# Kernel optimization log

Measured on AMD Instinct MI355X. Metric: run time of the kernel, lower is better.

The kernel has to match this reference:

```python
import jax, jax.numpy as jnp
import numpy as np

N, NODE_DIM, EDGE_DIM, HID, NREL = 1024, 128, 32, 128, 16


def _sage(h, adj, W, b):
    # agg = mean over (weighted) neighbors: (adj @ h) / (deg + 1e-6)
    agg = (adj @ h) / (jnp.sum(adj, axis=1, keepdims=True) + 1e-6)
    return jax.nn.relu(jnp.concatenate([h, agg], axis=1) @ W.T + b)


def setup_inputs() -> dict:
    key = jax.random.key(0)
    ks = jax.random.split(key, 12)
    s1 = 1.0 / np.sqrt(2 * NODE_DIM)
    s2 = 1.0 / np.sqrt(2 * HID)
    s3 = 1.0 / np.sqrt(2 * HID + EDGE_DIM)
    s4 = 1.0 / np.sqrt(HID)
    return {
        "node_feat": jax.random.normal(ks[0], (N, NODE_DIM), jnp.float32),
        "edge_feat": jax.random.normal(ks[1], (N, N, EDGE_DIM), jnp.float32),
        "adj": jax.random.uniform(ks[2], (N, N), jnp.float32),
        "W_g1": jax.random.normal(ks[3], (HID, 2 * NODE_DIM), jnp.float32) * s1,
        "b_g1": jax.random.normal(ks[4], (HID,), jnp.float32) * s1,
        "W_g2": jax.random.normal(ks[5], (HID, 2 * HID), jnp.float32) * s2,
        "b_g2": jax.random.normal(ks[6], (HID,), jnp.float32) * s2,
        "W_c1": jax.random.normal(ks[7], (HID, 2 * HID + EDGE_DIM), jnp.float32) * s3,
        "b_c1": jax.random.normal(ks[8], (HID,), jnp.float32) * s3,
        "W_c2": jax.random.normal(ks[9], (NREL, HID), jnp.float32) * s4,
        "b_c2": jax.random.normal(ks[10], (NREL,), jnp.float32) * s4,
    }


def reference(node_feat, edge_feat, adj, W_g1, b_g1, W_g2, b_g2, W_c1, b_c1, W_c2, b_c2):
    h = _sage(node_feat, adj, W_g1, b_g1)          # [N, HID]
    h = _sage(h, adj, W_g2, b_g2)                  # [N, HID]
    H = h.shape[1]
    # Split first classifier layer over [h_i ; h_j ; e_ij] to avoid a huge concat.
    Wa, Wb, We = W_c1[:, :H], W_c1[:, H:2 * H], W_c1[:, 2 * H:]
    pre = ((h @ Wa.T)[:, None, :]
           + (h @ Wb.T)[None, :, :]
           + jnp.einsum('ije,he->ijh', edge_feat, We)
           + b_c1)                                  # [N, N, HID]
    logits = jax.nn.relu(pre) @ W_c2.T + b_c2       # [N, N, NREL]
    # diagonal (i == j) stays zero, matching the skipped loop iterations
    n = logits.shape[0]
    mask = 1.0 - jnp.eye(n, dtype=logits.dtype)
    return logits * mask[:, :, None]
```

## Files before the change

### kernel.cpp

```cpp
#include <hip/hip_runtime.h>
#include <hip/hip_bf16.h>
#include <stdint.h>

constexpr int NN = 1024;
constexpr int DD = 128;
constexpr int EDIM = 32;
constexpr int NR = 16;

using short4v = __attribute__((ext_vector_type(4))) short;
using short8v = __attribute__((ext_vector_type(8))) short;
using f32x4   = __attribute__((ext_vector_type(4))) float;

__device__ __forceinline__ short f2bf(float x) {
  __hip_bfloat16 h = __float2bfloat16(x);
  return __builtin_bit_cast(short, h);
}

__device__ __forceinline__ void nt_store4(float* p, const float4& v) {
  f32x4 t;
  t[0] = v.x; t[1] = v.y; t[2] = v.z; t[3] = v.w;
  __builtin_nontemporal_store(t, (f32x4*)p);
}

__device__ __forceinline__ void gl_lds16(const void* g, void* l) {
  __builtin_amdgcn_global_load_lds(
      (const __attribute__((address_space(1))) unsigned int*)(uintptr_t)g,
      (__attribute__((address_space(3))) unsigned int*)(uint32_t)(uintptr_t)l,
      16, 0, 0);
}

__global__ __launch_bounds__(256) void k_adjgemm(const float* __restrict__ adj,
                                                 const float* __restrict__ X,
                                                 float* __restrict__ part) {
  __shared__ float sadj[16][136];
  int t = threadIdx.x;
  int ic = blockIdx.x & 63, kc = blockIdx.x >> 6;
  int i0 = ic * 16, k0 = kc * 128;
  {
    int il = t >> 4;
    int kl = (t & 15) * 8;
    const float4* src = (const float4*)(adj + (size_t)(i0 + il) * NN + k0 + kl);
    *(float4*)&sadj[il][kl]     = src[0];
    *(float4*)&sadj[il][kl + 4] = src[1];
  }
  __syncthreads();
  int hq = (t & 31) * 4;
  int ir = t >> 5;
  float4 acc0 = {0,0,0,0}, acc1 = {0,0,0,0};
  const float* Xb = X + (size_t)k0 * DD + hq;
  #pragma unroll 4
  for (int k = 0; k < 128; ++k) {
    float4 xv = *(const float4*)(Xb + (size_t)k * DD);
    float a0 = sadj[ir][k];
    float a1 = sadj[ir + 8][k];
    acc0.x += a0 * xv.x; acc0.y += a0 * xv.y; acc0.z += a0 * xv.z; acc0.w += a0 * xv.w;
    acc1.x += a1 * xv.x; acc1.y += a1 * xv.y; acc1.z += a1 * xv.z; acc1.w += a1 * xv.w;
  }
  *(float4*)(part + ((size_t)kc * NN + (i0 + ir)) * DD + hq)     = acc0;
  *(float4*)(part + ((size_t)kc * NN + (i0 + ir + 8)) * DD + hq) = acc1;
}

__global__ __launch_bounds__(256) void k_dense1(const float* __restrict__ X,
                                                const float* __restrict__ part,
                                                const float* __restrict__ adj,
                                                const float* __restrict__ W,
                                                const float* __restrict__ b,
                                                float* __restrict__ out,
                                                float* __restrict__ rsinv) {
  __shared__ float sagg[2][128];
  __shared__ float red[4];
  int t = threadIdx.x;
  int ig = t >> 7, h = t & 127;
  int i = blockIdx.x * 2 + ig;
  {
    const float4* ar = (const float4*)(adj + (size_t)i * NN);
    float4 v0 = ar[h * 2], v1 = ar[h * 2 + 1];
    float s = v0.x + v0.y + v0.z + v0.w + v1.x + v1.y + v1.z + v1.w;
    #pragma unroll
    for (int off = 32; off > 0; off >>= 1) s += __shfl_down(s, off, 64);
    if ((t & 63) == 0) red[t >> 6] = s;
  }
  __syncthreads();
  float rs = 1.0f / (red[ig * 2] + red[ig * 2 + 1] + 1e-6f);
  if (h == 0) rsinv[i] = rs;
  {
    float ss = 0.f;
    #pragma unroll
    for (int kc = 0; kc < 8; ++kc) ss += part[(size_t)kc * NN * DD + (size_t)i * DD + h];
    sagg[ig][h] = ss * rs;
  }
  __syncthreads();
  const float4* xr = (const float4*)(X + (size_t)i * DD);
  const float4* ar = (const float4*)(&sagg[ig][0]);
  const float4* w1 = (const float4*)(W + (size_t)h * 256);
  const float4* w2 = (const float4*)(W + (size_t)h * 256 + DD);
  float acc = b[h];
  #pragma unroll 8
  for (int k = 0; k < 32; ++k) {
    float4 x = xr[k], w = w1[k];
    acc += x.x * w.x + x.y * w.y + x.z * w.z + x.w * w.w;
  }
  #pragma unroll 8
  for (int k = 0; k < 32; ++k) {
    float4 y = ar[k], w = w2[k];
    acc += y.x * w.x + y.y * w.y + y.z * w.z + y.w * w.w;
  }
  out[(size_t)i * DD + h] = fmaxf(acc, 0.f);
}

__global__ __launch_bounds__(256) void k_dense2ab(const float* __restrict__ X,
                                                  const float* __restrict__ part,
                                                  const float* __restrict__ rsinv,
                                                  const float* __restrict__ W,
                                                  const float* __restrict__ b,
                                                  const float* __restrict__ Wc1,
                                                  const float* __restrict__ bc1,
                                                  float* __restrict__ Aib,
                                                  float* __restrict__ Bmat) {
  __shared__ float sagg[2][128];
  __shared__ float sh2[2][128];
  int t = threadIdx.x;
  int ig = t >> 7, h = t & 127;
  int i = blockIdx.x * 2 + ig;
  {
    float ss = 0.f;
    #pragma unroll
    for (int kc = 0; kc < 8; ++kc) ss += part[(size_t)kc * NN * DD + (size_t)i * DD + h];
    sagg[ig][h] = ss * rsinv[i];
  }
  __syncthreads();
  {
    const float4* xr = (const float4*)(X + (size_t)i * DD);
    const float4* ar = (const float4*)(&sagg[ig][0]);
    const float4* w1 = (const float4*)(W + (size_t)h * 256);
    const float4* w2 = (const float4*)(W + (size_t)h * 256 + DD);
    float acc = b[h];
    #pragma unroll 8
    for (int k = 0; k < 32; ++k) {
      float4 x = xr[k], w = w1[k];
      acc += x.x * w.x + x.y * w.y + x.z * w.z + x.w * w.w;
    }
    #pragma unroll 8
    for (int k = 0; k < 32; ++k) {
      float4 y = ar[k], w = w2[k];
      acc += y.x * w.x + y.y * w.y + y.z * w.z + y.w * w.w;
    }
    sh2[ig][h] = fmaxf(acc, 0.f);
  }
  __syncthreads();
  const float4* xr = (const float4*)(&sh2[ig][0]);
  const float4* wa = (const float4*)(Wc1 + (size_t)h * 288);
  const float4* wb = (const float4*)(Wc1 + (size_t)h * 288 + 128);
  float aa = bc1[h], bb = 0.f;
  #pragma unroll 8
  for (int k = 0; k < 32; ++k) {
    float4 x = xr[k];
    float4 a = wa[k], b2 = wb[k];
    aa += x.x * a.x + x.y * a.y + x.z * a.z + x.w * a.w;
    bb += x.x * b2.x + x.y * b2.y + x.z * b2.z + x.w * b2.w;
  }
  Aib[(size_t)i * DD + h] = aa;
  Bmat[(size_t)i * DD + h] = bb;
}


#define EDGE_BODY(T, OFF, VMN, PF) do {                                       \
    float4 e0_, e1_;                                                          \
    asm volatile("s_waitcnt vmcnt(" #VMN ")\n\t"                              \
                 "ds_read_b128 %0, %2 offset:" #OFF "\n\t"                    \
                 "ds_read_b128 %1, %3 offset:" #OFF "\n\t"                    \
                 "s_waitcnt lgkmcnt(0)"                                       \
                 : "=&v"(e0_), "=&v"(e1_)                                     \
                 : "v"(ea0), "v"(ea1)                                         \
                 : "memory");                                                 \
    __builtin_amdgcn_sched_barrier(0);                                        \
    if (PF) {                                                                 \
      const char* src_ = ebl + (size_t)((T) + 5) * 131072;                    \
      gl_lds16(src_, esw + (OFF));                                            \
      gl_lds16(src_ + 1024, esw + (OFF) + 1024);                              \
    }                                                                         \
    __builtin_amdgcn_sched_barrier(0);                                        \
    short8v ef_;                                                              \
    ef_[0]=f2bf(e0_.x); ef_[1]=f2bf(e0_.y); ef_[2]=f2bf(e0_.z); ef_[3]=f2bf(e0_.w); \
    ef_[4]=f2bf(e1_.x); ef_[5]=f2bf(e1_.y); ef_[6]=f2bf(e1_.z); ef_[7]=f2bf(e1_.w); \
    char* pw_ = psm + (((T) & 1) << 12);                                      \
    const float* ap_ = aibs + (T) * 128 + 4 * g;                              \
    _Pragma("unroll")                                                         \
    for (int n = 0; n < 8; ++n) {                                             \
      float4 av_ = *(const float4*)(ap_ + 16 * n);                            \
      f32x4 ci_;                                                              \
      ci_[0] = av_.x + bjv[n].x; ci_[1] = av_.y + bjv[n].y;                   \
      ci_[2] = av_.z + bjv[n].z; ci_[3] = av_.w + bjv[n].w;                   \
      f32x4 acc_ = __builtin_amdgcn_mfma_f32_16x16x32_bf16(weF[n], ef_, ci_, 0, 0, 0); \
      short4v pk_;                                                            \
      pk_[0] = f2bf(fmaxf(acc_[0], 0.f)); pk_[1] = f2bf(fmaxf(acc_[1], 0.f)); \
      pk_[2] = f2bf(fmaxf(acc_[2], 0.f)); pk_[3] = f2bf(fmaxf(acc_[3], 0.f)); \
      *(short4v*)(pw_ + (((n >> 1) << 10) + ((n & 1) << 9) + wroff)) = pk_;   \
    }                                                                         \
  } while (0)

#define G2(G2T, OREG) do {                                                    \
    f32x4 a2_;                                                                \
    a2_[0] = bc2v.x; a2_[1] = bc2v.y; a2_[2] = bc2v.z; a2_[3] = bc2v.w;       \
    const char* pp_ = psm + (((G2T) & 1) << 12);                              \
    _Pragma("unroll")                                                         \
    for (int kk = 0; kk < 4; ++kk) {                                          \
      short8v pb_ = *(const short8v*)(pp_ + ((kk << 10) + rdP));              \
      a2_ = __builtin_amdgcn_mfma_f32_16x16x32_bf16(wcF[kk], pb_, a2_, 0, 0, 0); \
    }                                                                         \
    bool dg_ = (j == i0 + (G2T));                                             \
    OREG.x = dg_ ? 0.f : a2_[0];                                              \
    OREG.y = dg_ ? 0.f : a2_[1];                                              \
    OREG.z = dg_ ? 0.f : a2_[2];                                              \
    OREG.w = dg_ ? 0.f : a2_[3];                                              \
  } while (0)

#define FLUSH(BASE) do {                                                      \
    nt_store4(out + ((size_t)(i0 + (BASE) + 0) * NN + j) * NR + 4 * g, o0);   \
    nt_store4(out + ((size_t)(i0 + (BASE) + 1) * NN + j) * NR + 4 * g, o1);   \
    nt_store4(out + ((size_t)(i0 + (BASE) + 2) * NN + j) * NR + 4 * g, o2);   \
    nt_store4(out + ((size_t)(i0 + (BASE) + 3) * NN + j) * NR + 4 * g, o3);   \
  } while (0)

__global__ __launch_bounds__(256, 2) void k_edge(const float* __restrict__ edge,
                                                 const float* __restrict__ Wc1,
                                                 const float* __restrict__ Wc2,
                                                 const float* __restrict__ bc2,
                                                 const float* __restrict__ Aib,
                                                 const float* __restrict__ Bmat,
                                                 float* __restrict__ out) {
  __shared__ __align__(16) char esm[4][5][2048];
  __shared__ __align__(16) char psm_all[4][2][4096];
  __shared__ __align__(16) float aibs[16 * 128];
  int tid = threadIdx.x;
  int w = tid >> 6, lane = tid & 63;
  int c = lane & 15, g = lane >> 4;
  int ig = blockIdx.x >> 4, jg = blockIdx.x & 15;
  int i0 = ig * 16;
  int j0w = jg * 64 + w * 16;
  int j = j0w + c;

  {
    int ii = tid >> 4, h8 = (tid & 15) * 8;
    const float4* s = (const float4*)(Aib + (size_t)(i0 + ii) * DD + h8);
    *(float4*)(aibs + ii * 128 + h8)     = s[0];
    *(float4*)(aibs + ii * 128 + h8 + 4) = s[1];
  }

  short8v weF[8];
  #pragma unroll
  for (int n = 0; n < 8; ++n) {
    const float* p = Wc1 + (size_t)(16 * n + c) * 288 + 256 + 8 * g;
    float4 f0 = *(const float4*)p;
    float4 f1 = *(const float4*)(p + 4);
    short8v s;
    s[0]=f2bf(f0.x); s[1]=f2bf(f0.y); s[2]=f2bf(f0.z); s[3]=f2bf(f0.w);
    s[4]=f2bf(f1.x); s[5]=f2bf(f1.y); s[6]=f2bf(f1.z); s[7]=f2bf(f1.w);
    weF[n] = s;
  }
  short8v wcF[4];
  #pragma unroll
  for (int kk = 0; kk < 4; ++kk) {
    const float* p = Wc2 + (size_t)c * DD + 32 * kk + 8 * g;
    float4 f0 = *(const float4*)p;
    float4 f1 = *(const float4*)(p + 4);
    short8v s;
    s[0]=f2bf(f0.x); s[1]=f2bf(f0.y); s[2]=f2bf(f0.z); s[3]=f2bf(f0.w);
    s[4]=f2bf(f1.x); s[5]=f2bf(f1.y); s[6]=f2bf(f1.z); s[7]=f2bf(f1.w);
    wcF[kk] = s;
  }
  float4 bc2v = *(const float4*)(bc2 + 4 * g);
  float4 bjv[8];
  #pragma unroll
  for (int n = 0; n < 8; ++n)
    bjv[n] = *(const float4*)(Bmat + (size_t)j * DD + 16 * n + 4 * g);

  __syncthreads();

  char* esw = &esm[w][0][0];
  char* psm = &psm_all[w][0][0];
  const char* ebl = (const char*)edge + ((size_t)i0 * NN + j0w) * (EDIM * 4)
                    + ((lane * 16) ^ (((lane >> 3) & 7) << 4));
  int rd0 = c * 128 + ((g * 32)      ^ ((c & 7) << 4));
  int rd1 = c * 128 + ((g * 32 + 16) ^ ((c & 7) << 4));
  int ldsb = (int)(uint32_t)(uintptr_t)esw;
  int ea0 = ldsb + rd0;
  int ea1 = ldsb + rd1;
  int wroff = (c << 4) + ((g & 1) << 3) + ((g >> 1) << 8);
  int rdP   = (g << 8) + (c << 4);

  float4 o0, o1, o2, o3;

  gl_lds16(ebl,                      esw);
  gl_lds16(ebl + 1024,               esw + 1024);
  gl_lds16(ebl + 1 * 131072,         esw + 2048);
  gl_lds16(ebl + 1 * 131072 + 1024,  esw + 3072);
  gl_lds16(ebl + 2 * 131072,         esw + 4096);
  gl_lds16(ebl + 2 * 131072 + 1024,  esw + 5120);
  gl_lds16(ebl + 3 * 131072,         esw + 6144);
  gl_lds16(ebl + 3 * 131072 + 1024,  esw + 7168);
  gl_lds16(ebl + 4 * 131072,         esw + 8192);
  gl_lds16(ebl + 4 * 131072 + 1024,  esw + 9216);

  EDGE_BODY(0,  0,    8, 1);
  EDGE_BODY(1,  2048, 8, 1);  G2(0, o0);
  EDGE_BODY(2,  4096, 8, 1);  G2(1, o1);
  EDGE_BODY(3,  6144, 8, 1);  G2(2, o2);
  EDGE_BODY(4,  8192, 8, 1);  G2(3, o3);  FLUSH(0);
  EDGE_BODY(5,  0,    12, 1); G2(4, o0);
  EDGE_BODY(6,  2048, 12, 1); G2(5, o1);
  EDGE_BODY(7,  4096, 12, 1); G2(6, o2);
  EDGE_BODY(8,  6144, 12, 1); G2(7, o3);  FLUSH(4);
  EDGE_BODY(9,  8192, 12, 1); G2(8, o0);
  EDGE_BODY(10, 0,    12, 1); G2(9, o1);
  EDGE_BODY(11, 2048, 12, 0); G2(10, o2);
  EDGE_BODY(12, 4096, 10, 0); G2(11, o3); FLUSH(8);
  EDGE_BODY(13, 6144, 12, 0); G2(12, o0);
  EDGE_BODY(14, 8192, 6, 0);  G2(13, o1);
  EDGE_BODY(15, 0,    4, 0);  G2(14, o2);
  G2(15, o3); FLUSH(12);
}

extern "C" void kernel_launch(void* const* d_in, const int* in_sizes, int n_in,
                              void* d_out, int out_size, void* d_ws, size_t ws_size,
                              hipStream_t stream) {
  const float* node_feat = (const float*)d_in[0];
  const float* edge_feat = (const float*)d_in[1];
  const float* adj  = (const float*)d_in[2];
  const float* W_g1 = (const float*)d_in[3];
  const float* b_g1 = (const float*)d_in[4];
  const float* W_g2 = (const float*)d_in[5];
  const float* b_g2 = (const float*)d_in[6];
  const float* W_c1 = (const float*)d_in[7];
  const float* b_c1 = (const float*)d_in[8];
  const float* W_c2 = (const float*)d_in[9];
  const float* b_c2 = (const float*)d_in[10];
  float* out = (float*)d_out;

  float* ws    = (float*)d_ws;
  float* rsinv = ws;
  float* part  = ws + 1024;
  float* h1    = part + 8 * NN * DD;
  float* Aib   = h1 + NN * DD;
  float* Bmat  = Aib + NN * DD;

  k_adjgemm<<<512, 256, 0, stream>>>(adj, node_feat, part);
  k_dense1<<<512, 256, 0, stream>>>(node_feat, part, adj, W_g1, b_g1, h1, rsinv);
  k_adjgemm<<<512, 256, 0, stream>>>(adj, h1, part);
  k_dense2ab<<<512, 256, 0, stream>>>(h1, part, rsinv, W_g2, b_g2, W_c1, b_c1, Aib, Bmat);
  k_edge<<<1024, 256, 0, stream>>>(edge_feat, W_c1, W_c2, b_c2, Aib, Bmat, out);
}
```

Measured before the change: 127.8 us.

## Replace LDS-staged edge feature loads with register-prefetched global loads

The edge kernel used to stage edge features into LDS with asynchronous global_load_lds, behind a 5-deep ring and hand-written vmcnt waits and swizzled ds_reads. Now each lane loads its own two float4s straight into registers, keeping a 6-deep rotating register prefetch. This removes the LDS round trip, the inline asm and about 40 KB of LDS per block, which may help occupancy. In exchange it needs more VGPRs, hands wait scheduling to the compiler, and each lane now reads 32 contiguous bytes of a 128-byte row, which may coalesce differently.

```diff
diff --git a/kernel.cpp b/kernel.cpp
--- a/kernel.cpp
+++ b/kernel.cpp
@@ -20,13 +20,6 @@
   f32x4 t;
   t[0] = v.x; t[1] = v.y; t[2] = v.z; t[3] = v.w;
   __builtin_nontemporal_store(t, (f32x4*)p);
-}
-
-__device__ __forceinline__ void gl_lds16(const void* g, void* l) {
-  __builtin_amdgcn_global_load_lds(
-      (const __attribute__((address_space(1))) unsigned int*)(uintptr_t)g,
-      (__attribute__((address_space(3))) unsigned int*)(uint32_t)(uintptr_t)l,
-      16, 0, 0);
 }
 
 __global__ __launch_bounds__(256) void k_adjgemm(const float* __restrict__ adj,
@@ -164,25 +157,16 @@
 }
 
 
-#define EDGE_BODY(T, OFF, VMN, PF) do {                                       \
-    float4 e0_, e1_;                                                          \
-    asm volatile("s_waitcnt vmcnt(" #VMN ")\n\t"                              \
-                 "ds_read_b128 %0, %2 offset:" #OFF "\n\t"                    \
-                 "ds_read_b128 %1, %3 offset:" #OFF "\n\t"                    \
-                 "s_waitcnt lgkmcnt(0)"                                       \
-                 : "=&v"(e0_), "=&v"(e1_)                                     \
-                 : "v"(ea0), "v"(ea1)                                         \
-                 : "memory");                                                 \
-    __builtin_amdgcn_sched_barrier(0);                                        \
+#define EDGE_BODY(T, S, PF) do {                                              \
+    float4 a_ = eA##S, b_ = eB##S;                                            \
     if (PF) {                                                                 \
-      const char* src_ = ebl + (size_t)((T) + 5) * 131072;                    \
-      gl_lds16(src_, esw + (OFF));                                            \
-      gl_lds16(src_ + 1024, esw + (OFF) + 1024);                              \
+      const float* p_ = ebl + (size_t)((T) + 6) * ((size_t)NN * EDIM);        \
+      eA##S = *(const float4*)p_;                                             \
+      eB##S = *(const float4*)(p_ + 4);                                       \
     }                                                                         \
-    __builtin_amdgcn_sched_barrier(0);                                        \
     short8v ef_;                                                              \
-    ef_[0]=f2bf(e0_.x); ef_[1]=f2bf(e0_.y); ef_[2]=f2bf(e0_.z); ef_[3]=f2bf(e0_.w); \
-    ef_[4]=f2bf(e1_.x); ef_[5]=f2bf(e1_.y); ef_[6]=f2bf(e1_.z); ef_[7]=f2bf(e1_.w); \
+    ef_[0]=f2bf(a_.x); ef_[1]=f2bf(a_.y); ef_[2]=f2bf(a_.z); ef_[3]=f2bf(a_.w); \
+    ef_[4]=f2bf(b_.x); ef_[5]=f2bf(b_.y); ef_[6]=f2bf(b_.z); ef_[7]=f2bf(b_.w); \
     char* pw_ = psm + (((T) & 1) << 12);                                      \
     const float* ap_ = aibs + (T) * 128 + 4 * g;                              \
     _Pragma("unroll")                                                         \
@@ -229,7 +213,6 @@
                                                  const float* __restrict__ Aib,
                                                  const float* __restrict__ Bmat,
                                                  float* __restrict__ out) {
-  __shared__ __align__(16) char esm[4][5][2048];
   __shared__ __align__(16) char psm_all[4][2][4096];
   __shared__ __align__(16) float aibs[16 * 128];
   int tid = threadIdx.x;
@@ -277,47 +260,40 @@
 
   __syncthreads();
 
-  char* esw = &esm[w][0][0];
   char* psm = &psm_all[w][0][0];
-  const char* ebl = (const char*)edge + ((size_t)i0 * NN + j0w) * (EDIM * 4)
-                    + ((lane * 16) ^ (((lane >> 3) & 7) << 4));
-  int rd0 = c * 128 + ((g * 32)      ^ ((c & 7) << 4));
-  int rd1 = c * 128 + ((g * 32 + 16) ^ ((c & 7) << 4));
-  int ldsb = (int)(uint32_t)(uintptr_t)esw;
-  int ea0 = ldsb + rd0;
-  int ea1 = ldsb + rd1;
+  const float* ebl = edge + ((size_t)i0 * NN + j) * EDIM + 8 * g;
   int wroff = (c << 4) + ((g & 1) << 3) + ((g >> 1) << 8);
   int rdP   = (g << 8) + (c << 4);
 
   float4 o0, o1, o2, o3;
 
-  gl_lds16(ebl,                      esw);
-  gl_lds16(ebl + 1024,               esw + 1024);
-  gl_lds16(ebl + 1 * 131072,         esw + 2048);
-  gl_lds16(ebl + 1 * 131072 + 1024,  esw + 3072);
-  gl_lds16(ebl + 2 * 131072,         esw + 4096);
-  gl_lds16(ebl + 2 * 131072 + 1024,  esw + 5120);
-  gl_lds16(ebl + 3 * 131072,         esw + 6144);
-  gl_lds16(ebl + 3 * 131072 + 1024,  esw + 7168);
-  gl_lds16(ebl + 4 * 131072,         esw + 8192);
-  gl_lds16(ebl + 4 * 131072 + 1024,  esw + 9216);
-
-  EDGE_BODY(0,  0,    8, 1);
-  EDGE_BODY(1,  2048, 8, 1);  G2(0, o0);
-  EDGE_BODY(2,  4096, 8, 1);  G2(1, o1);
-  EDGE_BODY(3,  6144, 8, 1);  G2(2, o2);
-  EDGE_BODY(4,  8192, 8, 1);  G2(3, o3);  FLUSH(0);
-  EDGE_BODY(5,  0,    12, 1); G2(4, o0);
-  EDGE_BODY(6,  2048, 12, 1); G2(5, o1);
-  EDGE_BODY(7,  4096, 12, 1); G2(6, o2);
-  EDGE_BODY(8,  6144, 12, 1); G2(7, o3);  FLUSH(4);
-  EDGE_BODY(9,  8192, 12, 1); G2(8, o0);
-  EDGE_BODY(10, 0,    12, 1); G2(9, o1);
-  EDGE_BODY(11, 2048, 12, 0); G2(10, o2);
-  EDGE_BODY(12, 4096, 10, 0); G2(11, o3); FLUSH(8);
-  EDGE_BODY(13, 6144, 12, 0); G2(12, o0);
-  EDGE_BODY(14, 8192, 6, 0);  G2(13, o1);
-  EDGE_BODY(15, 0,    4, 0);  G2(14, o2);
+  float4 eA0, eB0, eA1, eB1, eA2, eB2, eA3, eB3, eA4, eB4, eA5, eB5;
+  {
+    const size_t STP = (size_t)NN * EDIM;
+    eA0 = *(const float4*)(ebl);            eB0 = *(const float4*)(ebl + 4);
+    eA1 = *(const float4*)(ebl + STP);      eB1 = *(const float4*)(ebl + STP + 4);
+    eA2 = *(const float4*)(ebl + 2 * STP);  eB2 = *(const float4*)(ebl + 2 * STP + 4);
+    eA3 = *(const float4*)(ebl + 3 * STP);  eB3 = *(const float4*)(ebl + 3 * STP + 4);
+    eA4 = *(const float4*)(ebl + 4 * STP);  eB4 = *(const float4*)(ebl + 4 * STP + 4);
+    eA5 = *(const float4*)(ebl + 5 * STP);  eB5 = *(const float4*)(ebl + 5 * STP + 4);
+  }
+
+  EDGE_BODY(0, 0, 1);
+  EDGE_BODY(1, 1, 1);  G2(0, o0);
+  EDGE_BODY(2, 2, 1);  G2(1, o1);
+  EDGE_BODY(3, 3, 1);  G2(2, o2);
+  EDGE_BODY(4, 4, 1);  G2(3, o3);  FLUSH(0);
+  EDGE_BODY(5, 5, 1);  G2(4, o0);
+  EDGE_BODY(6, 0, 1);  G2(5, o1);
+  EDGE_BODY(7, 1, 1);  G2(6, o2);
+  EDGE_BODY(8, 2, 1);  G2(7, o3);  FLUSH(4);
+  EDGE_BODY(9, 3, 1);  G2(8, o0);
+  EDGE_BODY(10, 4, 0); G2(9, o1);
+  EDGE_BODY(11, 5, 0); G2(10, o2);
+  EDGE_BODY(12, 0, 0); G2(11, o3); FLUSH(8);
+  EDGE_BODY(13, 1, 0); G2(12, o0);
+  EDGE_BODY(14, 2, 0); G2(13, o1);
+  EDGE_BODY(15, 3, 0); G2(14, o2);
   G2(15, o3); FLUSH(12);
 }
 
```

Result: no change. 125.6 us (-1.7%).
